# Kernel tuning notes

Hardware: AMD Instinct MI355X
Metric: run time of the kernel (lower is better)

Reference implementation:

```python
import jax, jax.numpy as jnp
import numpy as np

N_HEADS = 16
D_HEAD = 64  # embed_dim // n_heads = 1024 // 16


def setup_inputs() -> dict:
    key = jax.random.key(0)
    ks = jax.random.split(key, 8)
    B, S, E = 2, 2048, 1024
    return {
        "k_in": jax.random.normal(ks[0], (B, S, E), jnp.float32),
        "q_in": jax.random.normal(ks[1], (B, S, E), jnp.float32),
        "v_in": jax.random.normal(ks[2], (B, S, E), jnp.float32),
        "Wq": jax.random.normal(ks[3], (D_HEAD, D_HEAD), jnp.float32) / np.sqrt(D_HEAD),
        "Wk": jax.random.normal(ks[4], (D_HEAD, D_HEAD), jnp.float32) / np.sqrt(D_HEAD),
        "Wv": jax.random.normal(ks[5], (D_HEAD, D_HEAD), jnp.float32) / np.sqrt(D_HEAD),
        "Wo": jax.random.normal(ks[6], (E, E), jnp.float32) / np.sqrt(E),
        "bo": jnp.zeros((E,), jnp.float32),
    }


def reference(k_in, q_in, v_in, Wq, Wk, Wv, Wo, bo):
    B, Sq, E = q_in.shape
    Sk = k_in.shape[1]
    H, Dh = N_HEADS, D_HEAD
    # split heads: [B, S, H, Dh]
    q = q_in.reshape(B, Sq, H, Dh)
    k = k_in.reshape(B, Sk, H, Dh)
    v = v_in.reshape(B, Sk, H, Dh)
    # per-head linear projections (nn.Linear: x @ W.T), then [B, H, S, Dh]
    q = jnp.einsum("bshd,ed->bhse", q, Wq)
    k = jnp.einsum("bshd,ed->bhse", k, Wk)
    v = jnp.einsum("bshd,ed->bhse", v, Wv)
    # scaled dot-product attention
    scores = jnp.einsum("bhqd,bhkd->bhqk", q, k) / jnp.sqrt(jnp.asarray(Dh, q.dtype))
    attn = jax.nn.softmax(scores, axis=-1)
    ctx = jnp.einsum("bhqk,bhkd->bqhd", attn, v)  # [B, Sq, H, Dh]
    concat = ctx.reshape(B, Sq, H * Dh)
    return concat @ Wo.T + bo
```

## Files before the change

kernel.cpp:

```cpp
#include <hip/hip_runtime.h>
#include <hip/hip_fp16.h>

typedef _Float16 f16;
typedef _Float16 f16x8 __attribute__((ext_vector_type(8)));
typedef _Float16 f16x4v __attribute__((ext_vector_type(4)));
typedef float f32x4 __attribute__((ext_vector_type(4)));

#define B_ 2
#define S_ 2048
#define E_ 1024
#define H_ 16
#define DH_ 64

__device__ __forceinline__ f32x4 mfma16(f16x8 a, f16x8 b, f32x4 c) {
    return __builtin_amdgcn_mfma_f32_16x16x32_f16(a, b, c, 0, 0, 0);
}

__device__ __forceinline__ f16x8 cvt8(const float* p) {
    float4 v0 = *(const float4*)p;
    float4 v1 = *(const float4*)(p + 4);
    f16x8 r;
    r[0] = (f16)v0.x; r[1] = (f16)v0.y; r[2] = (f16)v0.z; r[3] = (f16)v0.w;
    r[4] = (f16)v1.x; r[5] = (f16)v1.y; r[6] = (f16)v1.z; r[7] = (f16)v1.w;
    return r;
}

__global__ __launch_bounds__(256) void proj_kernel(
    const float* __restrict__ q_in, const float* __restrict__ k_in,
    const float* __restrict__ v_in,
    const float* __restrict__ Wq, const float* __restrict__ Wk,
    const float* __restrict__ Wv,
    f16* __restrict__ Qg, f16* __restrict__ Kg, f16* __restrict__ Vt)
{
    int tid = threadIdx.x;
    int lane = tid & 63, wv = tid >> 6;
    int wid = blockIdx.x * 4 + wv;
    int proj = wid >> 12;
    int r = wid & 4095;
    int bh = r >> 7;
    int stile = r & 127;
    int sbase = stile * 16;
    int h = bh & 15;
    int b = bh >> 4;
    int c = lane & 15, g = lane >> 4;

    const float* x; const float* W;
    if (proj == 0)      { x = q_in; W = Wq; }
    else if (proj == 1) { x = k_in; W = Wk; }
    else                { x = v_in; W = Wv; }

    const float* xrow = x + (((size_t)(b * S_ + sbase + c) * H_ + h) << 6);
    f16x8 a0 = cvt8(xrow + g * 8);
    f16x8 a1 = cvt8(xrow + 32 + g * 8);

    f32x4 acc[4] = {};
#pragma unroll
    for (int nt = 0; nt < 4; ++nt) {
        const float* wrow = W + ((nt * 16 + c) << 6);
        f16x8 b0 = cvt8(wrow + g * 8);
        f16x8 b1 = cvt8(wrow + 32 + g * 8);
        acc[nt] = mfma16(a0, b0, acc[nt]);
        acc[nt] = mfma16(a1, b1, acc[nt]);
    }

    if (proj < 2) {
        f16* out = (proj == 0) ? Qg : Kg;
#pragma unroll
        for (int nt = 0; nt < 4; ++nt)
#pragma unroll
            for (int j = 0; j < 4; ++j) {
                int s = sbase + g * 4 + j;
                out[((size_t)bh * S_ + s) * DH_ + nt * 16 + c] = (f16)acc[nt][j];
            }
    } else {
#pragma unroll
        for (int nt = 0; nt < 4; ++nt) {
            f16x4v pk;
            pk[0] = (f16)acc[nt][0]; pk[1] = (f16)acc[nt][1];
            pk[2] = (f16)acc[nt][2]; pk[3] = (f16)acc[nt][3];
            *(f16x4v*)&Vt[((size_t)bh * DH_ + nt * 16 + c) * S_ + sbase + g * 4] = pk;
        }
    }
}

__global__ __launch_bounds__(256) void cvt_wo(const float* __restrict__ W,
                                              f16* __restrict__ out)
{
    int i = blockIdx.x * 256 + threadIdx.x;
    float4 v = *(const float4*)(W + (size_t)i * 4);
    f16x4v o;
    o[0] = (f16)v.x; o[1] = (f16)v.y; o[2] = (f16)v.z; o[3] = (f16)v.w;
    *(f16x4v*)(out + (size_t)i * 4) = o;
}

#define C1_ 0.18033688011112042f

__global__ __launch_bounds__(512, 4) void attn_kernel(
    const f16* __restrict__ Qg, const f16* __restrict__ Kg,
    const f16* __restrict__ Vt, f16* __restrict__ ctx)
{
    __shared__ __align__(16) f16 Kl[2][64 * 64];
    __shared__ __align__(16) f16 Vl[2][64 * 64];
    __shared__ __align__(16) f16 Pl[8][16 * 64];

    int tid = threadIdx.x, lane = tid & 63, wv = tid >> 6;
    int bx = blockIdx.x;
    int bh = bx >> 4, qt = bx & 15;
    int b = bh >> 4, h = bh & 15;
    int qbase = qt * 128 + wv * 16;
    int c = lane & 15, g = lane >> 4;
    int swz = (c & 7) << 3;

    const f16* Qh = Qg + (size_t)bh * S_ * DH_;
    const f16* Kh = Kg + (size_t)bh * S_ * DH_;
    const f16* Vh = Vt + (size_t)bh * DH_ * S_;

    int srow = tid >> 3, scc = tid & 7;
    int sdst = srow * 64 + ((scc * 8) ^ ((srow & 7) << 3));
    const f16* ksrc = Kh + (size_t)srow * DH_ + scc * 8;
    const f16* vsrc = Vh + (size_t)srow * S_ + scc * 8;

    f16x8 qf[2];
#pragma unroll
    for (int hh = 0; hh < 2; ++hh)
        qf[hh] = *(const f16x8*)(Qh + (size_t)(qbase + c) * DH_ + hh * 32 + g * 8);

    float m2 = -1e30f, lr = 0.f;
    f32x4 accO[4] = {};

    f16x8 kreg = *(const f16x8*)ksrc;
    f16x8 vreg = *(const f16x8*)vsrc;
    *(f16x8*)&Kl[0][sdst] = kreg;
    *(f16x8*)&Vl[0][sdst] = vreg;
    __syncthreads();

    int cur = 0;
#pragma unroll 1
    for (int kt = 0; kt < 32; ++kt) {
        if (kt < 31) {
            kreg = *(const f16x8*)(ksrc + (size_t)(kt + 1) * 64 * DH_);
            vreg = *(const f16x8*)(vsrc + (kt + 1) * 64);
        }

        const f16* KA = &Kl[cur][0];
        const f16* VA = &Vl[cur][0];

        f32x4 accS[4] = {};
#pragma unroll
        for (int ks = 0; ks < 4; ++ks) {
            f16x8 k0 = *(const f16x8*)&KA[(ks * 16 + c) * 64 + ((8 * g) ^ swz)];
            f16x8 k1 = *(const f16x8*)&KA[(ks * 16 + c) * 64 + ((32 + 8 * g) ^ swz)];
            accS[ks] = mfma16(k0, qf[0], accS[ks]);
            accS[ks] = mfma16(k1, qf[1], accS[ks]);
        }

        float rmax = fmaxf(fmaxf(accS[0][0], accS[0][1]),
                           fmaxf(accS[0][2], accS[0][3]));
#pragma unroll
        for (int ks = 1; ks < 4; ++ks)
#pragma unroll
            for (int j = 0; j < 4; ++j) rmax = fmaxf(rmax, accS[ks][j]);
        rmax = fmaxf(rmax, __shfl_xor(rmax, 16));
        rmax = fmaxf(rmax, __shfl_xor(rmax, 32));
        float pm2 = rmax * C1_;

        float al = 1.f;
        if (!__all(pm2 - m2 <= 8.f)) {
            float mn = fmaxf(m2, pm2);
            al = exp2f(m2 - mn);
            m2 = mn;
#pragma unroll
            for (int j = 0; j < 4; ++j) {
                float aj = __shfl(al, 4 * g + j);
#pragma unroll
                for (int nt = 0; nt < 4; ++nt) accO[nt][j] *= aj;
            }
        }

        float rs = 0.f;
        float p[4][4];
#pragma unroll
        for (int ks = 0; ks < 4; ++ks)
#pragma unroll
            for (int j = 0; j < 4; ++j) {
                float pv = exp2f(fmaf(accS[ks][j], C1_, -m2));
                p[ks][j] = pv; rs += pv;
            }
        rs += __shfl_xor(rs, 16);
        rs += __shfl_xor(rs, 32);
        lr = lr * al + rs;

#pragma unroll
        for (int ks = 0; ks < 4; ++ks) {
            f16x4v w;
            w[0] = (f16)p[ks][0]; w[1] = (f16)p[ks][1];
            w[2] = (f16)p[ks][2]; w[3] = (f16)p[ks][3];
            *(f16x4v*)&Pl[wv][c * 64 + ((16 * ks + 4 * g) ^ swz)] = w;
        }

#pragma unroll
        for (int kh = 0; kh < 2; ++kh) {
            f16x8 pa = *(const f16x8*)&Pl[wv][c * 64 + ((32 * kh + 8 * g) ^ swz)];
#pragma unroll
            for (int nt = 0; nt < 4; ++nt) {
                f16x8 vb = *(const f16x8*)&VA[(nt * 16 + c) * 64
                                              + ((32 * kh + 8 * g) ^ swz)];
                accO[nt] = mfma16(pa, vb, accO[nt]);
            }
        }

        if (kt < 31) {
            *(f16x8*)&Kl[cur ^ 1][sdst] = kreg;
            *(f16x8*)&Vl[cur ^ 1][sdst] = vreg;
            __syncthreads();
        }
        cur ^= 1;
    }

    float inv = 1.f / lr;
#pragma unroll
    for (int j = 0; j < 4; ++j) {
        float lj = __shfl(inv, 4 * g + j);
        int s = qbase + 4 * g + j;
#pragma unroll
        for (int nt = 0; nt < 4; ++nt)
            ctx[((size_t)b * S_ + s) * E_ + h * DH_ + nt * 16 + c] =
                (f16)(accO[nt][j] * lj);
    }
}

__global__ __launch_bounds__(256) void gemm_out(
    const f16* __restrict__ A,
    const f16* __restrict__ Bw,
    const float* __restrict__ bo,
    float* __restrict__ out)
{
    __shared__ __align__(16) f16 Al[2][128 * 64];
    __shared__ __align__(16) f16 Bl[2][64 * 64];

    int tid = threadIdx.x, lane = tid & 63, wv = tid >> 6;
    int mbase = blockIdx.x * 128, nbase = blockIdx.y * 64;
    int c = lane & 15, g = lane >> 4;
    int wr = wv >> 1, wc = wv & 1;
    int swz = (c & 7) << 3;

    int arow[4], adst[4]; const f16* asrc[4];
#pragma unroll
    for (int i = 0; i < 4; ++i) {
        int slot = tid + i * 256;
        arow[i] = slot >> 3;
        int cc = slot & 7;
        adst[i] = arow[i] * 64 + ((cc * 8) ^ ((arow[i] & 7) << 3));
        asrc[i] = A + (size_t)(mbase + arow[i]) * 1024 + cc * 8;
    }
    int bdst[2]; const f16* bsrc[2];
#pragma unroll
    for (int i = 0; i < 2; ++i) {
        int slot = tid + i * 256;
        int row = slot >> 3, cc = slot & 7;
        bdst[i] = row * 64 + ((cc * 8) ^ ((row & 7) << 3));
        bsrc[i] = Bw + (size_t)(nbase + row) * 1024 + cc * 8;
    }

    f32x4 acc[4][2] = {};

    f16x8 areg[4], breg[2];
#pragma unroll
    for (int i = 0; i < 4; ++i) areg[i] = *(const f16x8*)asrc[i];
#pragma unroll
    for (int i = 0; i < 2; ++i) breg[i] = *(const f16x8*)bsrc[i];
#pragma unroll
    for (int i = 0; i < 4; ++i) *(f16x8*)&Al[0][adst[i]] = areg[i];
#pragma unroll
    for (int i = 0; i < 2; ++i) *(f16x8*)&Bl[0][bdst[i]] = breg[i];
    __syncthreads();

    int cur = 0;
#pragma unroll 1
    for (int ks = 0; ks < 16; ++ks) {
        if (ks < 15) {
#pragma unroll
            for (int i = 0; i < 4; ++i)
                areg[i] = *(const f16x8*)(asrc[i] + (ks + 1) * 64);
#pragma unroll
            for (int i = 0; i < 2; ++i)
                breg[i] = *(const f16x8*)(bsrc[i] + (ks + 1) * 64);
        }

        const f16* AA = &Al[cur][0];
        const f16* BB = &Bl[cur][0];
#pragma unroll
        for (int kk = 0; kk < 2; ++kk) {
            f16x8 af[4], bf[2];
#pragma unroll
            for (int mi = 0; mi < 4; ++mi)
                af[mi] = *(const f16x8*)&AA[(wr * 64 + mi * 16 + c) * 64
                                            + ((32 * kk + 8 * g) ^ swz)];
#pragma unroll
            for (int ni = 0; ni < 2; ++ni)
                bf[ni] = *(const f16x8*)&BB[(wc * 32 + ni * 16 + c) * 64
                                            + ((32 * kk + 8 * g) ^ swz)];
#pragma unroll
            for (int mi = 0; mi < 4; ++mi)
#pragma unroll
                for (int ni = 0; ni < 2; ++ni)
                    acc[mi][ni] = mfma16(af[mi], bf[ni], acc[mi][ni]);
        }

        if (ks < 15) {
#pragma unroll
            for (int i = 0; i < 4; ++i) *(f16x8*)&Al[cur ^ 1][adst[i]] = areg[i];
#pragma unroll
            for (int i = 0; i < 2; ++i) *(f16x8*)&Bl[cur ^ 1][bdst[i]] = breg[i];
            __syncthreads();
        }
        cur ^= 1;
    }

#pragma unroll
    for (int ni = 0; ni < 2; ++ni) {
        float bias = bo[nbase + wc * 32 + ni * 16 + c];
#pragma unroll
        for (int mi = 0; mi < 4; ++mi)
#pragma unroll
            for (int j = 0; j < 4; ++j) {
                int m = mbase + wr * 64 + mi * 16 + g * 4 + j;
                out[(size_t)m * 1024 + nbase + wc * 32 + ni * 16 + c] =
                    acc[mi][ni][j] + bias;
            }
    }
}

extern "C" void kernel_launch(void* const* d_in, const int* in_sizes, int n_in,
                              void* d_out, int out_size, void* d_ws, size_t ws_size,
                              hipStream_t stream)
{
    const float* k_in = (const float*)d_in[0];
    const float* q_in = (const float*)d_in[1];
    const float* v_in = (const float*)d_in[2];
    const float* Wq   = (const float*)d_in[3];
    const float* Wk   = (const float*)d_in[4];
    const float* Wv   = (const float*)d_in[5];
    const float* Wo   = (const float*)d_in[6];
    const float* bo   = (const float*)d_in[7];
    float* out = (float*)d_out;

    char* ws = (char*)d_ws;
    f16* Qg  = (f16*)(ws);
    f16* Kg  = (f16*)(ws + (8u << 20));
    f16* Vt  = (f16*)(ws + (16u << 20));
    f16* ctx = (f16*)(ws + (24u << 20));
    f16* WoH = (f16*)(ws + (32u << 20));

    proj_kernel<<<dim3(3072), dim3(256), 0, stream>>>(q_in, k_in, v_in,
                                                      Wq, Wk, Wv, Qg, Kg, Vt);
    cvt_wo<<<dim3(1024), dim3(256), 0, stream>>>(Wo, WoH);
    attn_kernel<<<dim3(512), dim3(512), 0, stream>>>(Qg, Kg, Vt, ctx);
    gemm_out<<<dim3(32, 16), dim3(256), 0, stream>>>(ctx, WoH, bo, out);
}
```

Measured before the change: 121.1 us.

## Widen attention K/V tiles, unroll double-buffer loops, add priorities and block swizzle

The attention kernel now stages 128 keys per shared-memory tile (two 64-key sub-steps), which halves the number of barriers. It also defers the cross-lane row-sum reduction until the end and shuffles the row max only when a rescale is needed. Both attention and the output GEMM unroll the double-buffer loop by two with constant buffer indices. MFMA sections are wrapped in s_setprio, and block IDs are remapped across XCDs to improve L2 locality. The larger LDS footprint (about 80KB per attention block) may lower occupancy under the launch bound of 4 blocks.

```diff
diff --git a/kernel.cpp b/kernel.cpp
--- a/kernel.cpp
+++ b/kernel.cpp
@@ -14,6 +14,13 @@
 
 __device__ __forceinline__ f32x4 mfma16(f16x8 a, f16x8 b, f32x4 c) {
     return __builtin_amdgcn_mfma_f32_16x16x32_f16(a, b, c, 0, 0, 0);
+}
+
+__device__ __forceinline__ f32x4 vmax4(f32x4 a, f32x4 b) {
+    f32x4 r;
+    r[0] = fmaxf(a[0], b[0]); r[1] = fmaxf(a[1], b[1]);
+    r[2] = fmaxf(a[2], b[2]); r[3] = fmaxf(a[3], b[3]);
+    return r;
 }
 
 __device__ __forceinline__ f16x8 cvt8(const float* p) {
@@ -99,13 +106,14 @@
     const f16* __restrict__ Qg, const f16* __restrict__ Kg,
     const f16* __restrict__ Vt, f16* __restrict__ ctx)
 {
-    __shared__ __align__(16) f16 Kl[2][64 * 64];
-    __shared__ __align__(16) f16 Vl[2][64 * 64];
+    __shared__ __align__(16) f16 Kl[2][128 * 64];
+    __shared__ __align__(16) f16 Vl[2][2][64 * 64];
     __shared__ __align__(16) f16 Pl[8][16 * 64];
 
     int tid = threadIdx.x, lane = tid & 63, wv = tid >> 6;
-    int bx = blockIdx.x;
-    int bh = bx >> 4, qt = bx & 15;
+    int bid = blockIdx.x;
+    int sb = (bid & 7) * 64 + (bid >> 3);
+    int bh = sb >> 4, qt = sb & 15;
     int b = bh >> 4, h = bh & 15;
     int qbase = qt * 128 + wv * 16;
     int c = lane & 15, g = lane >> 4;
@@ -115,108 +123,121 @@
     const f16* Kh = Kg + (size_t)bh * S_ * DH_;
     const f16* Vh = Vt + (size_t)bh * DH_ * S_;
 
-    int srow = tid >> 3, scc = tid & 7;
-    int sdst = srow * 64 + ((scc * 8) ^ ((srow & 7) << 3));
-    const f16* ksrc = Kh + (size_t)srow * DH_ + scc * 8;
-    const f16* vsrc = Vh + (size_t)srow * S_ + scc * 8;
+    int s0 = tid, s1 = tid + 512;
+    int kr0 = s0 >> 3, kc0 = s0 & 7, kr1 = s1 >> 3, kc1 = s1 & 7;
+    int kd0 = kr0 * 64 + ((kc0 * 8) ^ ((kr0 & 7) << 3));
+    int kd1 = kr1 * 64 + ((kc1 * 8) ^ ((kr1 & 7) << 3));
+    const f16* ksp0 = Kh + kr0 * 64 + kc0 * 8;
+    const f16* ksp1 = Kh + kr1 * 64 + kc1 * 8;
+    int vr0 = s0 >> 4, vc0 = s0 & 15, vr1 = s1 >> 4, vc1 = s1 & 15;
+    int vst0 = vc0 >> 3, vst1 = vc1 >> 3;
+    int vd0 = vr0 * 64 + (((vc0 & 7) * 8) ^ ((vr0 & 7) << 3));
+    int vd1 = vr1 * 64 + (((vc1 & 7) * 8) ^ ((vr1 & 7) << 3));
+    const f16* vsp0 = Vh + vr0 * S_ + vc0 * 8;
+    const f16* vsp1 = Vh + vr1 * S_ + vc1 * 8;
 
     f16x8 qf[2];
 #pragma unroll
     for (int hh = 0; hh < 2; ++hh)
         qf[hh] = *(const f16x8*)(Qh + (size_t)(qbase + c) * DH_ + hh * 32 + g * 8);
 
-    float m2 = -1e30f, lr = 0.f;
+    float m2 = -1e30f;
+    f32x4 lrv = {};
     f32x4 accO[4] = {};
-
-    f16x8 kreg = *(const f16x8*)ksrc;
-    f16x8 vreg = *(const f16x8*)vsrc;
-    *(f16x8*)&Kl[0][sdst] = kreg;
-    *(f16x8*)&Vl[0][sdst] = vreg;
+    f16x8 kreg0, kreg1, vreg0, vreg1;
+
+    kreg0 = *(const f16x8*)ksp0; kreg1 = *(const f16x8*)ksp1;
+    vreg0 = *(const f16x8*)vsp0; vreg1 = *(const f16x8*)vsp1;
+    *(f16x8*)&Kl[0][kd0] = kreg0; *(f16x8*)&Kl[0][kd1] = kreg1;
+    *(f16x8*)&Vl[0][vst0][vd0] = vreg0; *(f16x8*)&Vl[0][vst1][vd1] = vreg1;
     __syncthreads();
 
-    int cur = 0;
+#define ATTN_STEP(CUR, T, STAGE)                                               \
+    do {                                                                       \
+        if (STAGE) {                                                           \
+            int ko = ((T) + 1) * 128 * 64, vo = ((T) + 1) * 128;               \
+            kreg0 = *(const f16x8*)(ksp0 + ko);                                \
+            kreg1 = *(const f16x8*)(ksp1 + ko);                                \
+            vreg0 = *(const f16x8*)(vsp0 + vo);                                \
+            vreg1 = *(const f16x8*)(vsp1 + vo);                                \
+        }                                                                      \
+        _Pragma("unroll")                                                      \
+        for (int st = 0; st < 2; ++st) {                                       \
+            f32x4 accS[4] = {};                                                \
+            __builtin_amdgcn_s_setprio(1);                                     \
+            _Pragma("unroll")                                                  \
+            for (int ks = 0; ks < 4; ++ks) {                                   \
+                int krow = (st * 64 + ks * 16 + c) * 64;                       \
+                f16x8 k0 = *(const f16x8*)&Kl[CUR][krow + ((8 * g) ^ swz)];    \
+                f16x8 k1 = *(const f16x8*)&Kl[CUR][krow + ((32 + 8 * g) ^ swz)];\
+                accS[ks] = mfma16(k0, qf[0], accS[ks]);                        \
+                accS[ks] = mfma16(k1, qf[1], accS[ks]);                        \
+            }                                                                  \
+            __builtin_amdgcn_s_setprio(0);                                     \
+            f32x4 mx4 = vmax4(vmax4(accS[0], accS[1]), vmax4(accS[2], accS[3]));\
+            float rmax = fmaxf(fmaxf(mx4[0], mx4[1]), fmaxf(mx4[2], mx4[3]));  \
+            if (!__all(fmaf(rmax, C1_, -m2) <= 8.f)) {                         \
+                float mx = fmaxf(rmax, __shfl_xor(rmax, 16));                  \
+                mx = fmaxf(mx, __shfl_xor(mx, 32));                            \
+                float mn = fmaxf(m2, mx * C1_);                                \
+                float al = exp2f(m2 - mn);                                     \
+                m2 = mn;                                                       \
+                _Pragma("unroll")                                              \
+                for (int j = 0; j < 4; ++j) lrv[j] *= al;                      \
+                _Pragma("unroll")                                              \
+                for (int j = 0; j < 4; ++j) {                                  \
+                    float aj = __shfl(al, 4 * g + j);                          \
+                    _Pragma("unroll")                                          \
+                    for (int nt = 0; nt < 4; ++nt) accO[nt][j] *= aj;          \
+                }                                                              \
+            }                                                                  \
+            _Pragma("unroll")                                                  \
+            for (int ks = 0; ks < 4; ++ks) {                                   \
+                f32x4 e;                                                       \
+                _Pragma("unroll")                                              \
+                for (int j = 0; j < 4; ++j)                                    \
+                    e[j] = exp2f(fmaf(accS[ks][j], C1_, -m2));                 \
+                lrv += e;                                                      \
+                f16x4v w;                                                      \
+                w[0] = (f16)e[0]; w[1] = (f16)e[1];                            \
+                w[2] = (f16)e[2]; w[3] = (f16)e[3];                            \
+                *(f16x4v*)&Pl[wv][c * 64 + ((16 * ks + 4 * g) ^ swz)] = w;     \
+            }                                                                  \
+            __builtin_amdgcn_s_setprio(1);                                     \
+            _Pragma("unroll")                                                  \
+            for (int kh = 0; kh < 2; ++kh) {                                   \
+                f16x8 pa = *(const f16x8*)&Pl[wv][c * 64                       \
+                                + (((st * 64 + 32 * kh + 8 * g) & 63) ^ swz)]; \
+                _Pragma("unroll")                                              \
+                for (int nt = 0; nt < 4; ++nt) {                               \
+                    f16x8 vb = *(const f16x8*)&Vl[CUR][st][(nt * 16 + c) * 64  \
+                                    + ((32 * kh + 8 * g) ^ swz)];              \
+                    accO[nt] = mfma16(pa, vb, accO[nt]);                       \
+                }                                                              \
+            }                                                                  \
+            __builtin_amdgcn_s_setprio(0);                                     \
+        }                                                                      \
+        if (STAGE) {                                                           \
+            int nb = (CUR) ^ 1;                                                \
+            *(f16x8*)&Kl[nb][kd0] = kreg0; *(f16x8*)&Kl[nb][kd1] = kreg1;      \
+            *(f16x8*)&Vl[nb][vst0][vd0] = vreg0;                               \
+            *(f16x8*)&Vl[nb][vst1][vd1] = vreg1;                               \
+            __syncthreads();                                                   \
+        }                                                                      \
+    } while (0)
+
 #pragma unroll 1
-    for (int kt = 0; kt < 32; ++kt) {
-        if (kt < 31) {
-            kreg = *(const f16x8*)(ksrc + (size_t)(kt + 1) * 64 * DH_);
-            vreg = *(const f16x8*)(vsrc + (kt + 1) * 64);
-        }
-
-        const f16* KA = &Kl[cur][0];
-        const f16* VA = &Vl[cur][0];
-
-        f32x4 accS[4] = {};
-#pragma unroll
-        for (int ks = 0; ks < 4; ++ks) {
-            f16x8 k0 = *(const f16x8*)&KA[(ks * 16 + c) * 64 + ((8 * g) ^ swz)];
-            f16x8 k1 = *(const f16x8*)&KA[(ks * 16 + c) * 64 + ((32 + 8 * g) ^ swz)];
-            accS[ks] = mfma16(k0, qf[0], accS[ks]);
-            accS[ks] = mfma16(k1, qf[1], accS[ks]);
-        }
-
-        float rmax = fmaxf(fmaxf(accS[0][0], accS[0][1]),
-                           fmaxf(accS[0][2], accS[0][3]));
-#pragma unroll
-        for (int ks = 1; ks < 4; ++ks)
-#pragma unroll
-            for (int j = 0; j < 4; ++j) rmax = fmaxf(rmax, accS[ks][j]);
-        rmax = fmaxf(rmax, __shfl_xor(rmax, 16));
-        rmax = fmaxf(rmax, __shfl_xor(rmax, 32));
-        float pm2 = rmax * C1_;
-
-        float al = 1.f;
-        if (!__all(pm2 - m2 <= 8.f)) {
-            float mn = fmaxf(m2, pm2);
-            al = exp2f(m2 - mn);
-            m2 = mn;
-#pragma unroll
-            for (int j = 0; j < 4; ++j) {
-                float aj = __shfl(al, 4 * g + j);
-#pragma unroll
-                for (int nt = 0; nt < 4; ++nt) accO[nt][j] *= aj;
-            }
-        }
-
-        float rs = 0.f;
-        float p[4][4];
-#pragma unroll
-        for (int ks = 0; ks < 4; ++ks)
-#pragma unroll
-            for (int j = 0; j < 4; ++j) {
-                float pv = exp2f(fmaf(accS[ks][j], C1_, -m2));
-                p[ks][j] = pv; rs += pv;
-            }
-        rs += __shfl_xor(rs, 16);
-        rs += __shfl_xor(rs, 32);
-        lr = lr * al + rs;
-
-#pragma unroll
-        for (int ks = 0; ks < 4; ++ks) {
-            f16x4v w;
-            w[0] = (f16)p[ks][0]; w[1] = (f16)p[ks][1];
-            w[2] = (f16)p[ks][2]; w[3] = (f16)p[ks][3];
-            *(f16x4v*)&Pl[wv][c * 64 + ((16 * ks + 4 * g) ^ swz)] = w;
-        }
-
-#pragma unroll
-        for (int kh = 0; kh < 2; ++kh) {
-            f16x8 pa = *(const f16x8*)&Pl[wv][c * 64 + ((32 * kh + 8 * g) ^ swz)];
-#pragma unroll
-            for (int nt = 0; nt < 4; ++nt) {
-                f16x8 vb = *(const f16x8*)&VA[(nt * 16 + c) * 64
-                                              + ((32 * kh + 8 * g) ^ swz)];
-                accO[nt] = mfma16(pa, vb, accO[nt]);
-            }
-        }
-
-        if (kt < 31) {
-            *(f16x8*)&Kl[cur ^ 1][sdst] = kreg;
-            *(f16x8*)&Vl[cur ^ 1][sdst] = vreg;
-            __syncthreads();
-        }
-        cur ^= 1;
-    }
-
+    for (int kt = 0; kt < 14; kt += 2) {
+        ATTN_STEP(0, kt, 1);
+        ATTN_STEP(1, kt + 1, 1);
+    }
+    ATTN_STEP(0, 14, 1);
+    ATTN_STEP(1, 15, 0);
+#undef ATTN_STEP
+
+    float lr = (lrv[0] + lrv[1]) + (lrv[2] + lrv[3]);
+    lr += __shfl_xor(lr, 16);
+    lr += __shfl_xor(lr, 32);
     float inv = 1.f / lr;
 #pragma unroll
     for (int j = 0; j < 4; ++j) {
@@ -239,19 +260,20 @@
     __shared__ __align__(16) f16 Bl[2][64 * 64];
 
     int tid = threadIdx.x, lane = tid & 63, wv = tid >> 6;
-    int mbase = blockIdx.x * 128, nbase = blockIdx.y * 64;
+    int bid = blockIdx.x;
+    int sb = (bid & 7) * 64 + (bid >> 3);
+    int mbase = (sb & 31) * 128, nbase = (sb >> 5) * 64;
     int c = lane & 15, g = lane >> 4;
     int wr = wv >> 1, wc = wv & 1;
     int swz = (c & 7) << 3;
 
-    int arow[4], adst[4]; const f16* asrc[4];
+    int adst[4]; const f16* asrc[4];
 #pragma unroll
     for (int i = 0; i < 4; ++i) {
         int slot = tid + i * 256;
-        arow[i] = slot >> 3;
-        int cc = slot & 7;
-        adst[i] = arow[i] * 64 + ((cc * 8) ^ ((arow[i] & 7) << 3));
-        asrc[i] = A + (size_t)(mbase + arow[i]) * 1024 + cc * 8;
+        int row = slot >> 3, cc = slot & 7;
+        adst[i] = row * 64 + ((cc * 8) ^ ((row & 7) << 3));
+        asrc[i] = A + (size_t)(mbase + row) * 1024 + cc * 8;
     }
     int bdst[2]; const f16* bsrc[2];
 #pragma unroll
@@ -263,8 +285,8 @@
     }
 
     f32x4 acc[4][2] = {};
-
     f16x8 areg[4], breg[2];
+
 #pragma unroll
     for (int i = 0; i < 4; ++i) areg[i] = *(const f16x8*)asrc[i];
 #pragma unroll
@@ -275,47 +297,53 @@
     for (int i = 0; i < 2; ++i) *(f16x8*)&Bl[0][bdst[i]] = breg[i];
     __syncthreads();
 
-    int cur = 0;
+#define GEMM_STEP(CUR, T, STAGE)                                               \
+    do {                                                                       \
+        if (STAGE) {                                                           \
+            _Pragma("unroll")                                                  \
+            for (int i = 0; i < 4; ++i)                                        \
+                areg[i] = *(const f16x8*)(asrc[i] + ((T) + 1) * 64);           \
+            _Pragma("unroll")                                                  \
+            for (int i = 0; i < 2; ++i)                                        \
+                breg[i] = *(const f16x8*)(bsrc[i] + ((T) + 1) * 64);           \
+        }                                                                      \
+        __builtin_amdgcn_s_setprio(1);                                         \
+        _Pragma("unroll")                                                      \
+        for (int kk = 0; kk < 2; ++kk) {                                       \
+            f16x8 af[4], bf[2];                                                \
+            _Pragma("unroll")                                                  \
+            for (int mi = 0; mi < 4; ++mi)                                     \
+                af[mi] = *(const f16x8*)&Al[CUR][(wr * 64 + mi * 16 + c) * 64  \
+                                               + ((32 * kk + 8 * g) ^ swz)];   \
+            _Pragma("unroll")                                                  \
+            for (int ni = 0; ni < 2; ++ni)                                     \
+                bf[ni] = *(const f16x8*)&Bl[CUR][(wc * 32 + ni * 16 + c) * 64  \
+                                               + ((32 * kk + 8 * g) ^ swz)];   \
+            _Pragma("unroll")                                                  \
+            for (int mi = 0; mi < 4; ++mi)                                     \
+                _Pragma("unroll")                                              \
+                for (int ni = 0; ni < 2; ++ni)                                 \
+                    acc[mi][ni] = mfma16(af[mi], bf[ni], acc[mi][ni]);         \
+        }                                                                      \
+        __builtin_amdgcn_s_setprio(0);                                         \
+        if (STAGE) {                                                           \
+            int nb = (CUR) ^ 1;                                                \
+            _Pragma("unroll")                                                  \
+            for (int i = 0; i < 4; ++i) *(f16x8*)&Al[nb][adst[i]] = areg[i];   \
+            _Pragma("unroll")                                                  \
+            for (int i = 0; i < 2; ++i) *(f16x8*)&Bl[nb][bdst[i]] = breg[i];   \
+            __syncthreads();                                                   \
+        }                                                                      \
+    } while (0)
+
 #pragma unroll 1
-    for (int ks = 0; ks < 16; ++ks) {
-        if (ks < 15) {
-#pragma unroll
-            for (int i = 0; i < 4; ++i)
-                areg[i] = *(const f16x8*)(asrc[i] + (ks + 1) * 64);
-#pragma unroll
-            for (int i = 0; i < 2; ++i)
-                breg[i] = *(const f16x8*)(bsrc[i] + (ks + 1) * 64);
-        }
-
-        const f16* AA = &Al[cur][0];
-        const f16* BB = &Bl[cur][0];
-#pragma unroll
-        for (int kk = 0; kk < 2; ++kk) {
-            f16x8 af[4], bf[2];
-#pragma unroll
-            for (int mi = 0; mi < 4; ++mi)
-                af[mi] = *(const f16x8*)&AA[(wr * 64 + mi * 16 + c) * 64
-                                            + ((32 * kk + 8 * g) ^ swz)];
-#pragma unroll
-            for (int ni = 0; ni < 2; ++ni)
-                bf[ni] = *(const f16x8*)&BB[(wc * 32 + ni * 16 + c) * 64
-                                            + ((32 * kk + 8 * g) ^ swz)];
-#pragma unroll
-            for (int mi = 0; mi < 4; ++mi)
-#pragma unroll
-                for (int ni = 0; ni < 2; ++ni)
-                    acc[mi][ni] = mfma16(af[mi], bf[ni], acc[mi][ni]);
-        }
-
-        if (ks < 15) {
-#pragma unroll
-            for (int i = 0; i < 4; ++i) *(f16x8*)&Al[cur ^ 1][adst[i]] = areg[i];
-#pragma unroll
-            for (int i = 0; i < 2; ++i) *(f16x8*)&Bl[cur ^ 1][bdst[i]] = breg[i];
-            __syncthreads();
-        }
-        cur ^= 1;
-    }
+    for (int ks = 0; ks < 14; ks += 2) {
+        GEMM_STEP(0, ks, 1);
+        GEMM_STEP(1, ks + 1, 1);
+    }
+    GEMM_STEP(0, 14, 1);
+    GEMM_STEP(1, 15, 0);
+#undef GEMM_STEP
 
 #pragma unroll
     for (int ni = 0; ni < 2; ++ni) {
@@ -356,5 +384,5 @@
                                                       Wq, Wk, Wv, Qg, Kg, Vt);
     cvt_wo<<<dim3(1024), dim3(256), 0, stream>>>(Wo, WoH);
     attn_kernel<<<dim3(512), dim3(512), 0, stream>>>(Qg, Kg, Vt, ctx);
-    gemm_out<<<dim3(32, 16), dim3(256), 0, stream>>>(ctx, WoH, bo, out);
-}
+    gemm_out<<<dim3(512), dim3(256), 0, stream>>>(ctx, WoH, bo, out);
+}
```

Result: faster. 115.0 us (-5.0%).
